# Kernel tuning notes

Hardware: AMD Instinct MI355X
Metric: run time of the kernel (lower is better)

The kernel has to match this reference:

```python
import jax, jax.numpy as jnp
import numpy as np

EMBED, HEAD, CTX = 1024, 64, 2048

def setup_inputs() -> dict:
    key = jax.random.key(0)
    k1, k2, k3, k4 = jax.random.split(key, 4)
    x = jax.random.normal(k1, (16, 2048, EMBED), dtype=jnp.float32)
    s = EMBED ** -0.5  # torch Linear default init scale-ish
    Wq = jax.random.normal(k2, (EMBED, HEAD), dtype=jnp.float32) * s
    Wk = jax.random.normal(k3, (EMBED, HEAD), dtype=jnp.float32) * s
    Wv = jax.random.normal(k4, (EMBED, HEAD), dtype=jnp.float32) * s
    return {"x": x, "Wq": Wq, "Wk": Wk, "Wv": Wv}

def reference(x, Wq, Wk, Wv):
    # x: [B, S, E] -> q,k,v: [B, S, H]
    q = jnp.einsum('bse,eh->bsh', x, Wq)
    k = jnp.einsum('bse,eh->bsh', x, Wk)
    v = jnp.einsum('bse,eh->bsh', x, Wv)
    scale = k.shape[-1] ** -0.5
    scores = jnp.einsum('bqh,bkh->bqk', q, k) * scale  # [B, S, S]
    S = x.shape[1]
    causal = jnp.tril(jnp.ones((S, S), dtype=bool))
    scores = jnp.where(causal, scores, -jnp.inf)
    attn = jax.nn.softmax(scores, axis=-1)
    return jnp.einsum('bqk,bkh->bqh', attn, v)  # [B, S, H]
```

## Files before the change

### kernel.cpp

```cpp
#include <hip/hip_runtime.h>
#include <math.h>

#define BATCH 16
#define SEQ   2048
#define EMB   1024
#define HD    64
#define NROWS (BATCH*SEQ)

typedef __attribute__((ext_vector_type(8))) short short8;
typedef __attribute__((ext_vector_type(4))) float f32x4;

#define SWZ(byte, row)   ((byte) ^ (((row) & 7) << 4))
#define SWZ16(byte, row) ((byte) ^ (((row) & 15) << 4))

__device__ __forceinline__ ushort f2bf(float f) {
    union { float f; unsigned u; } c; c.f = f;
    return (ushort)((c.u + 0x7FFF + ((c.u >> 16) & 1)) >> 16);
}

__device__ __forceinline__ void gload_lds16(const void* g, void* l) {
    __builtin_amdgcn_global_load_lds(
        (const __attribute__((address_space(1))) void*)g,
        (__attribute__((address_space(3))) void*)l, 16, 0, 0);
}

__global__ void k_transpose_w(const float* __restrict__ Wq,
                              const float* __restrict__ Wk,
                              const float* __restrict__ Wv,
                              ushort* __restrict__ wt) {
    int idx  = blockIdx.x * 256 + threadIdx.x;
    int c192 = idx >> 10;
    int e    = idx & 1023;
    const float* W = (c192 < 64) ? Wq : (c192 < 128 ? Wk : Wv);
    wt[idx] = f2bf(W[e * HD + (c192 & 63)]);
}

__global__ __launch_bounds__(256)
void k_qkv_proj(const float* __restrict__ x, const ushort* __restrict__ wt,
                ushort* __restrict__ qkv, ushort* __restrict__ vt) {
    __shared__ short8 smem[49152 / 16];
    char* base = (char*)smem;
    const int t = threadIdx.x, lane = t & 63, w = t >> 6;
    const int l15 = lane & 15, lg = lane >> 4;
    const int row0 = blockIdx.x * 64;
    const float* xrowp = x + (size_t)(row0 + w * 16 + l15) * EMB;

    f32x4 acc[12];
    #pragma unroll
    for (int mi = 0; mi < 12; ++mi) acc[mi] = (f32x4){0.f, 0.f, 0.f, 0.f};

    float4 xc[4], xn[4];

    auto stage_w = [&](int ch, int buf) {
        char* wb = base + buf * 24576;
        #pragma unroll
        for (int i = 0; i < 6; ++i) {
            int r = (w * 6 + i) * 8 + (lane >> 3);
            int j = (lane & 7) ^ (r & 7);
            gload_lds16(&wt[(size_t)r * EMB + ch * 64 + j * 8],
                        wb + (w * 6 + i) * 1024);
        }
    };
    auto load_x = [&](int ch, float4* xr) {
        #pragma unroll
        for (int s = 0; s < 2; ++s) {
            const float* p = xrowp + ch * 64 + s * 32 + lg * 8;
            xr[s * 2 + 0] = *(const float4*)(p);
            xr[s * 2 + 1] = *(const float4*)(p + 4);
        }
    };

    stage_w(0, 0); load_x(0, xc);
    #pragma unroll 2
    for (int ch = 0; ch < 16; ++ch) {
        int cur = ch & 1;
        if (ch < 15) {
            stage_w(ch + 1, cur ^ 1); load_x(ch + 1, xn);
            asm volatile("s_waitcnt vmcnt(10)" ::: "memory");
        } else {
            asm volatile("s_waitcnt vmcnt(0)" ::: "memory");
        }
        __builtin_amdgcn_sched_barrier(0);
        __builtin_amdgcn_s_barrier();
        char* wb = base + cur * 24576;
        #pragma unroll
        for (int s = 0; s < 2; ++s) {
            const float* xp = (const float*)&xc[s * 2];
            short8 xf;
            #pragma unroll
            for (int e = 0; e < 8; ++e) xf[e] = (short)f2bf(xp[e]);
            __builtin_amdgcn_s_setprio(1);
            #pragma unroll
            for (int mi = 0; mi < 12; ++mi) {
                int cr = mi * 16 + l15;
                short8 wf = *(short8*)(wb + SWZ(cr * 128 + s * 64 + lg * 16, cr));
                acc[mi] = (mi < 8)
                    ? __builtin_amdgcn_mfma_f32_16x16x32_bf16(wf, xf, acc[mi], 0, 0, 0)
                    : __builtin_amdgcn_mfma_f32_16x16x32_bf16(xf, wf, acc[mi], 0, 0, 0);
            }
            __builtin_amdgcn_s_setprio(0);
        }
        if (ch < 15) {
            #pragma unroll
            for (int i = 0; i < 4; ++i) xc[i] = xn[i];
        }
        __builtin_amdgcn_sched_barrier(0);
        __builtin_amdgcn_s_barrier();
    }

    char* qkb = base;
    char* vtb = base + 16384;
    const float qscale = 0.125f * 1.44269504f;
    #pragma unroll
    for (int mi = 0; mi < 12; ++mi) {
        ushort4 o;
        if (mi < 8) {
            float sc = (mi < 4) ? qscale : 1.0f;
            o.x = f2bf(acc[mi][0] * sc); o.y = f2bf(acc[mi][1] * sc);
            o.z = f2bf(acc[mi][2] * sc); o.w = f2bf(acc[mi][3] * sc);
            int xrow = w * 16 + l15, c = mi * 16 + lg * 4;
            *(ushort4*)(qkb + SWZ16(xrow * 256 + c * 2, xrow)) = o;
        } else {
            o.x = f2bf(acc[mi][0]); o.y = f2bf(acc[mi][1]);
            o.z = f2bf(acc[mi][2]); o.w = f2bf(acc[mi][3]);
            int hd = (mi - 8) * 16 + l15, key = w * 16 + lg * 4;
            *(ushort4*)(vtb + SWZ(hd * 128 + key * 2, hd)) = o;
        }
    }
    __syncthreads();
    const int b = row0 >> 11, r0b = row0 & 2047;
    #pragma unroll
    for (int i = 0; i < 4; ++i) {
        int idx = t + i * 256;
        int r = idx >> 4, g = idx & 15;
        short8 v = *(short8*)(qkb + SWZ16(r * 256 + g * 16, r));
        int c0 = g * 8, m = c0 >> 6, c = c0 & 63;
        *(short8*)&qkv[((size_t)m * NROWS + row0 + r) * HD + c] = v;
    }
    #pragma unroll
    for (int i = 0; i < 2; ++i) {
        int idx = t + i * 256;
        int hd = idx >> 3, g = idx & 7;
        short8 v = *(short8*)(vtb + SWZ(hd * 128 + g * 16, hd));
        *(short8*)&vt[((size_t)b * HD + hd) * SEQ + r0b + g * 8] = v;
    }
}

__global__ __launch_bounds__(256)
void k_attn(const ushort* __restrict__ q, const ushort* __restrict__ k,
            const ushort* __restrict__ vt, float* __restrict__ out) {
    __shared__ short8 smem[81920 / 16];
    char* base = (char*)smem;
    char* pls  = base + 65536;
    const int t = threadIdx.x, lane = t & 63, w = t >> 6;
    const int l15 = lane & 15, lg = lane >> 4;
    const int b = blockIdx.x & 15, qt = 31 - (blockIdx.x >> 4);
    const int row0 = qt * 64, r0w = row0 + w * 16;
    const ushort* qb = q  + (size_t)b * SEQ * HD;
    const ushort* kb = k  + (size_t)b * SEQ * HD;
    const ushort* vb = vt + (size_t)b * HD * SEQ;
    char* pw = pls + w * 4096;

    short8 qf[2];
    #pragma unroll
    for (int s = 0; s < 2; ++s)
        qf[s] = *(const short8*)&qb[(size_t)(r0w + l15) * HD + s * 32 + lg * 8];

    f32x4 oacc[4];
    #pragma unroll
    for (int h = 0; h < 4; ++h) oacc[h] = (f32x4){0.f, 0.f, 0.f, 0.f};
    float m_ = -INFINITY, l_ = 0.f;

    auto stage = [&](int kt, int buf) {
        char* kbuf = base + buf * 32768;
        char* vbuf = kbuf + 16384;
        int k0 = kt * 128;
        #pragma unroll
        for (int g = 0; g < 4; ++g) {
            int rk = w * 32 + g * 8 + (lane >> 3);
            int jk = (lane & 7) ^ (rk & 7);
            gload_lds16(&kb[(size_t)(k0 + rk) * HD + jk * 8],
                        kbuf + (w * 4 + g) * 1024);
            int rv = w * 16 + g * 4 + (lane >> 4);
            int jv = (lane & 15) ^ (rv & 15);
            gload_lds16(&vb[(size_t)rv * SEQ + k0 + jv * 8],
                        vbuf + (w * 4 + g) * 1024);
        }
    };

    const int npair = (qt + 2) >> 1;
    stage(0, 0);
    for (int kt = 0; kt < npair; ++kt) {
        int cur = kt & 1;
        if (kt + 1 < npair) {
            stage(kt + 1, cur ^ 1);
            asm volatile("s_waitcnt vmcnt(8)" ::: "memory");
        } else {
            asm volatile("s_waitcnt vmcnt(0)" ::: "memory");
        }
        __builtin_amdgcn_sched_barrier(0);
        __builtin_amdgcn_s_barrier();
        char* kls = base + cur * 32768;
        char* vls = kls + 16384;
        int k0 = kt * 128;

        f32x4 sa[8];
        #pragma unroll
        for (int a = 0; a < 8; ++a) sa[a] = (f32x4){0.f, 0.f, 0.f, 0.f};
        __builtin_amdgcn_s_setprio(1);
        #pragma unroll
        for (int s = 0; s < 2; ++s)
            #pragma unroll
            for (int a = 0; a < 8; ++a) {
                int r = a * 16 + l15;
                short8 kf = *(short8*)(kls + SWZ(r * 128 + s * 64 + lg * 16, r));
                sa[a] = __builtin_amdgcn_mfma_f32_16x16x32_bf16(kf, qf[s], sa[a], 0, 0, 0);
            }
        __builtin_amdgcn_s_setprio(0);

        if (kt == npair - 1) {
            int qrow = r0w + l15;
            #pragma unroll
            for (int a = 0; a < 8; ++a)
                #pragma unroll
                for (int r = 0; r < 4; ++r)
                    if (k0 + a * 16 + lg * 4 + r > qrow) sa[a][r] = -INFINITY;
        }

        float smax = -INFINITY;
        #pragma unroll
        for (int a = 0; a < 8; ++a)
            #pragma unroll
            for (int r = 0; r < 4; ++r) smax = fmaxf(smax, sa[a][r]);
        smax = fmaxf(smax, __shfl_xor(smax, 16));
        smax = fmaxf(smax, __shfl_xor(smax, 32));
        if (!__all(smax - m_ <= 8.0f)) {
            float mn   = fmaxf(m_, smax);
            float corr = __builtin_amdgcn_exp2f(m_ - mn);
            l_ *= corr;
            #pragma unroll
            for (int h = 0; h < 4; ++h) oacc[h] *= corr;
            m_ = mn;
        }
        float p[32], ps = 0.f;
        #pragma unroll
        for (int a = 0; a < 8; ++a)
            #pragma unroll
            for (int r = 0; r < 4; ++r) {
                float pv = __builtin_amdgcn_exp2f(sa[a][r] - m_);
                p[a * 4 + r] = pv; ps += pv;
            }
        ps += __shfl_xor(ps, 16);
        ps += __shfl_xor(ps, 32);
        l_ += ps;

        #pragma unroll
        for (int a = 0; a < 8; ++a) {
            ushort4 pb;
            pb.x = f2bf(p[a * 4 + 0]); pb.y = f2bf(p[a * 4 + 1]);
            pb.z = f2bf(p[a * 4 + 2]); pb.w = f2bf(p[a * 4 + 3]);
            *(ushort4*)(pw + SWZ16(l15 * 256 + a * 32 + lg * 8, l15)) = pb;
        }

        __builtin_amdgcn_s_setprio(1);
        #pragma unroll
        for (int ki = 0; ki < 4; ++ki) {
            short8 pf = *(short8*)(pw + SWZ16(l15 * 256 + ki * 64 + lg * 16, l15));
            #pragma unroll
            for (int h = 0; h < 4; ++h) {
                int rr = h * 16 + l15;
                short8 vf = *(short8*)(vls + SWZ16(rr * 256 + ki * 64 + lg * 16, rr));
                oacc[h] = __builtin_amdgcn_mfma_f32_16x16x32_bf16(vf, pf, oacc[h], 0, 0, 0);
            }
        }
        __builtin_amdgcn_s_setprio(0);
        __builtin_amdgcn_sched_barrier(0);
        __builtin_amdgcn_s_barrier();
    }

    float inv = 1.0f / l_;
    #pragma unroll
    for (int h = 0; h < 4; ++h) {
        f32x4 v = oacc[h] * inv;
        int qr = w * 16 + l15;
        *(f32x4*)(base + SWZ16(qr * 256 + h * 64 + lg * 16, qr)) = v;
    }
    __syncthreads();
    #pragma unroll
    for (int i = 0; i < 4; ++i) {
        int idx = t + i * 256;
        int r = idx >> 4, g = idx & 15;
        f32x4 v = *(f32x4*)(base + SWZ16(r * 256 + g * 16, r));
        *(f32x4*)&out[((size_t)b * SEQ + row0 + r) * HD + g * 4] = v;
    }
}

extern "C" void kernel_launch(void* const* d_in, const int* in_sizes, int n_in,
                              void* d_out, int out_size, void* d_ws, size_t ws_size,
                              hipStream_t stream) {
    const float* x  = (const float*)d_in[0];
    const float* Wq = (const float*)d_in[1];
    const float* Wk = (const float*)d_in[2];
    const float* Wv = (const float*)d_in[3];
    float* out = (float*)d_out;
    ushort* ws = (ushort*)d_ws;
    ushort* wt16 = ws;
    ushort* qk16 = ws + 192 * 1024;
    ushort* vt16 = qk16 + (size_t)2 * NROWS * HD;

    k_transpose_w<<<768, 256, 0, stream>>>(Wq, Wk, Wv, wt16);
    k_qkv_proj  <<<NROWS / 64, 256, 0, stream>>>(x, wt16, qk16, vt16);
    k_attn      <<<BATCH * (SEQ / 64), 256, 0, stream>>>(
                    qk16, qk16 + (size_t)NROWS * HD, vt16, out);
}
```

Baseline: 69.94 us.

## Split KV tile across wave pairs with 32-row query fragments and merge partial softmax

Each wave now owns 32 query rows and half of each 128-key tile, instead of 16 rows and the full tile. Every K fragment read from LDS therefore feeds two MFMAs, which halves K LDS reads per MFMA and roughly halves the P write and read traffic per wave. The two key-half partial results (running max, sum and output accumulator) are merged at the end through LDS. This adds a final merge step and doubles the accumulator register state per wave, which may hurt occupancy. The causal mask now uses a -1e30 running-max init, so a fully masked half-tile stays numerically safe.

Result: slower. 71.44 us (+2.1%).

```diff
diff --git a/kernel.cpp b/kernel.cpp
--- a/kernel.cpp
+++ b/kernel.cpp
@@ -146,6 +146,7 @@
     }
 }
 
+#define MINF (-1e30f)
 __global__ __launch_bounds__(256)
 void k_attn(const ushort* __restrict__ q, const ushort* __restrict__ k,
             const ushort* __restrict__ vt, float* __restrict__ out) {
@@ -154,22 +155,28 @@
     char* pls  = base + 65536;
     const int t = threadIdx.x, lane = t & 63, w = t >> 6;
     const int l15 = lane & 15, lg = lane >> 4;
+    const int rw = w & 1, kh = w >> 1;
     const int b = blockIdx.x & 15, qt = 31 - (blockIdx.x >> 4);
-    const int row0 = qt * 64, r0w = row0 + w * 16;
+    const int row0 = qt * 64;
     const ushort* qb = q  + (size_t)b * SEQ * HD;
     const ushort* kb = k  + (size_t)b * SEQ * HD;
     const ushort* vb = vt + (size_t)b * HD * SEQ;
     char* pw = pls + w * 4096;
 
-    short8 qf[2];
-    #pragma unroll
-    for (int s = 0; s < 2; ++s)
-        qf[s] = *(const short8*)&qb[(size_t)(r0w + l15) * HD + s * 32 + lg * 8];
-
-    f32x4 oacc[4];
-    #pragma unroll
-    for (int h = 0; h < 4; ++h) oacc[h] = (f32x4){0.f, 0.f, 0.f, 0.f};
-    float m_ = -INFINITY, l_ = 0.f;
+    short8 qf[2][2];
+    #pragma unroll
+    for (int f = 0; f < 2; ++f)
+        #pragma unroll
+        for (int s = 0; s < 2; ++s)
+            qf[f][s] = *(const short8*)&qb[(size_t)(row0 + rw * 32 + f * 16 + l15) * HD
+                                           + s * 32 + lg * 8];
+
+    f32x4 oacc[2][4];
+    #pragma unroll
+    for (int f = 0; f < 2; ++f)
+        #pragma unroll
+        for (int h = 0; h < 4; ++h) oacc[f][h] = (f32x4){0.f, 0.f, 0.f, 0.f};
+    float m_[2] = {MINF, MINF}, l_[2] = {0.f, 0.f};
 
     auto stage = [&](int kt, int buf) {
         char* kbuf = base + buf * 32768;
@@ -204,73 +211,89 @@
         char* vls = kls + 16384;
         int k0 = kt * 128;
 
-        f32x4 sa[8];
-        #pragma unroll
-        for (int a = 0; a < 8; ++a) sa[a] = (f32x4){0.f, 0.f, 0.f, 0.f};
+        f32x4 sa[2][4];
+        #pragma unroll
+        for (int f = 0; f < 2; ++f)
+            #pragma unroll
+            for (int a = 0; a < 4; ++a) sa[f][a] = (f32x4){0.f, 0.f, 0.f, 0.f};
         __builtin_amdgcn_s_setprio(1);
         #pragma unroll
         for (int s = 0; s < 2; ++s)
             #pragma unroll
-            for (int a = 0; a < 8; ++a) {
-                int r = a * 16 + l15;
+            for (int a = 0; a < 4; ++a) {
+                int r = kh * 64 + a * 16 + l15;
                 short8 kf = *(short8*)(kls + SWZ(r * 128 + s * 64 + lg * 16, r));
-                sa[a] = __builtin_amdgcn_mfma_f32_16x16x32_bf16(kf, qf[s], sa[a], 0, 0, 0);
+                sa[0][a] = __builtin_amdgcn_mfma_f32_16x16x32_bf16(kf, qf[0][s], sa[0][a], 0, 0, 0);
+                sa[1][a] = __builtin_amdgcn_mfma_f32_16x16x32_bf16(kf, qf[1][s], sa[1][a], 0, 0, 0);
             }
         __builtin_amdgcn_s_setprio(0);
 
         if (kt == npair - 1) {
-            int qrow = r0w + l15;
-            #pragma unroll
-            for (int a = 0; a < 8; ++a)
+            #pragma unroll
+            for (int f = 0; f < 2; ++f) {
+                int qrow = row0 + rw * 32 + f * 16 + l15;
+                #pragma unroll
+                for (int a = 0; a < 4; ++a)
+                    #pragma unroll
+                    for (int r = 0; r < 4; ++r)
+                        if (k0 + kh * 64 + a * 16 + lg * 4 + r > qrow)
+                            sa[f][a][r] = -INFINITY;
+            }
+        }
+
+        #pragma unroll
+        for (int f = 0; f < 2; ++f) {
+            float ma[4];
+            #pragma unroll
+            for (int a = 0; a < 4; ++a)
+                ma[a] = fmaxf(fmaxf(sa[f][a][0], sa[f][a][1]),
+                              fmaxf(sa[f][a][2], sa[f][a][3]));
+            float mx = fmaxf(fmaxf(ma[0], ma[1]), fmaxf(ma[2], ma[3]));
+            mx = fmaxf(mx, __shfl_xor(mx, 16));
+            mx = fmaxf(mx, __shfl_xor(mx, 32));
+            if (!__all(mx - m_[f] <= 8.0f)) {
+                float mn   = fmaxf(m_[f], mx);
+                float corr = __builtin_amdgcn_exp2f(m_[f] - mn);
+                l_[f] *= corr;
+                #pragma unroll
+                for (int h = 0; h < 4; ++h) oacc[f][h] *= corr;
+                m_[f] = mn;
+            }
+            float p[16];
+            #pragma unroll
+            for (int a = 0; a < 4; ++a)
                 #pragma unroll
                 for (int r = 0; r < 4; ++r)
-                    if (k0 + a * 16 + lg * 4 + r > qrow) sa[a][r] = -INFINITY;
-        }
-
-        float smax = -INFINITY;
-        #pragma unroll
-        for (int a = 0; a < 8; ++a)
-            #pragma unroll
-            for (int r = 0; r < 4; ++r) smax = fmaxf(smax, sa[a][r]);
-        smax = fmaxf(smax, __shfl_xor(smax, 16));
-        smax = fmaxf(smax, __shfl_xor(smax, 32));
-        if (!__all(smax - m_ <= 8.0f)) {
-            float mn   = fmaxf(m_, smax);
-            float corr = __builtin_amdgcn_exp2f(m_ - mn);
-            l_ *= corr;
-            #pragma unroll
-            for (int h = 0; h < 4; ++h) oacc[h] *= corr;
-            m_ = mn;
-        }
-        float p[32], ps = 0.f;
-        #pragma unroll
-        for (int a = 0; a < 8; ++a)
-            #pragma unroll
-            for (int r = 0; r < 4; ++r) {
-                float pv = __builtin_amdgcn_exp2f(sa[a][r] - m_);
-                p[a * 4 + r] = pv; ps += pv;
-            }
-        ps += __shfl_xor(ps, 16);
-        ps += __shfl_xor(ps, 32);
-        l_ += ps;
-
-        #pragma unroll
-        for (int a = 0; a < 8; ++a) {
-            ushort4 pb;
-            pb.x = f2bf(p[a * 4 + 0]); pb.y = f2bf(p[a * 4 + 1]);
-            pb.z = f2bf(p[a * 4 + 2]); pb.w = f2bf(p[a * 4 + 3]);
-            *(ushort4*)(pw + SWZ16(l15 * 256 + a * 32 + lg * 8, l15)) = pb;
+                    p[a * 4 + r] = __builtin_amdgcn_exp2f(sa[f][a][r] - m_[f]);
+            float s01 = (p[0] + p[1]) + (p[2] + p[3]);
+            float s23 = (p[4] + p[5]) + (p[6] + p[7]);
+            float s45 = (p[8] + p[9]) + (p[10] + p[11]);
+            float s67 = (p[12] + p[13]) + (p[14] + p[15]);
+            float ps = (s01 + s23) + (s45 + s67);
+            ps += __shfl_xor(ps, 16);
+            ps += __shfl_xor(ps, 32);
+            l_[f] += ps;
+            #pragma unroll
+            for (int a = 0; a < 4; ++a) {
+                ushort4 pb;
+                pb.x = f2bf(p[a * 4 + 0]); pb.y = f2bf(p[a * 4 + 1]);
+                pb.z = f2bf(p[a * 4 + 2]); pb.w = f2bf(p[a * 4 + 3]);
+                int prow = f * 16 + l15;
+                *(ushort4*)(pw + SWZ(prow * 128 + a * 32 + lg * 8, prow)) = pb;
+            }
         }
 
         __builtin_amdgcn_s_setprio(1);
         #pragma unroll
-        for (int ki = 0; ki < 4; ++ki) {
-            short8 pf = *(short8*)(pw + SWZ16(l15 * 256 + ki * 64 + lg * 16, l15));
+        for (int ki = 0; ki < 2; ++ki) {
+            short8 pf0 = *(short8*)(pw + SWZ((0 * 16 + l15) * 128 + ki * 64 + lg * 16, 0 * 16 + l15));
+            short8 pf1 = *(short8*)(pw + SWZ((1 * 16 + l15) * 128 + ki * 64 + lg * 16, 1 * 16 + l15));
             #pragma unroll
             for (int h = 0; h < 4; ++h) {
                 int rr = h * 16 + l15;
-                short8 vf = *(short8*)(vls + SWZ16(rr * 256 + ki * 64 + lg * 16, rr));
-                oacc[h] = __builtin_amdgcn_mfma_f32_16x16x32_bf16(vf, pf, oacc[h], 0, 0, 0);
+                short8 vf = *(short8*)(vls + SWZ16(rr * 256 + kh * 128 + ki * 64 + lg * 16, rr));
+                oacc[0][h] = __builtin_amdgcn_mfma_f32_16x16x32_bf16(vf, pf0, oacc[0][h], 0, 0, 0);
+                oacc[1][h] = __builtin_amdgcn_mfma_f32_16x16x32_bf16(vf, pf1, oacc[1][h], 0, 0, 0);
             }
         }
         __builtin_amdgcn_s_setprio(0);
@@ -278,20 +301,36 @@
         __builtin_amdgcn_s_barrier();
     }
 
-    float inv = 1.0f / l_;
-    #pragma unroll
-    for (int h = 0; h < 4; ++h) {
-        f32x4 v = oacc[h] * inv;
-        int qr = w * 16 + l15;
-        *(f32x4*)(base + SWZ16(qr * 256 + h * 64 + lg * 16, qr)) = v;
+    char* obuf = base + rw * 8192;
+    float* ml  = (float*)(base + 16384 + rw * 256);
+    if (kh == 1) {
+        #pragma unroll
+        for (int f = 0; f < 2; ++f) {
+            int prow = f * 16 + l15;
+            #pragma unroll
+            for (int h = 0; h < 4; ++h)
+                *(f32x4*)(obuf + SWZ16(prow * 256 + (h * 16 + lg * 4) * 4, prow)) = oacc[f][h];
+            if (lg == 0) { ml[prow] = m_[f]; ml[32 + prow] = l_[f]; }
+        }
     }
     __syncthreads();
-    #pragma unroll
-    for (int i = 0; i < 4; ++i) {
-        int idx = t + i * 256;
-        int r = idx >> 4, g = idx & 15;
-        f32x4 v = *(f32x4*)(base + SWZ16(r * 256 + g * 16, r));
-        *(f32x4*)&out[((size_t)b * SEQ + row0 + r) * HD + g * 4] = v;
+    if (kh == 0) {
+        #pragma unroll
+        for (int f = 0; f < 2; ++f) {
+            int prow = f * 16 + l15;
+            float m2 = ml[prow], l2 = ml[32 + prow];
+            float M  = fmaxf(m_[f], m2);
+            float s1 = __builtin_amdgcn_exp2f(m_[f] - M);
+            float s2 = __builtin_amdgcn_exp2f(m2 - M);
+            float inv = 1.0f / (l_[f] * s1 + l2 * s2);
+            int qrow = row0 + rw * 32 + prow;
+            #pragma unroll
+            for (int h = 0; h < 4; ++h) {
+                f32x4 o2 = *(f32x4*)(obuf + SWZ16(prow * 256 + (h * 16 + lg * 4) * 4, prow));
+                f32x4 o  = (oacc[f][h] * s1 + o2 * s2) * inv;
+                *(f32x4*)&out[((size_t)b * SEQ + qrow) * HD + h * 16 + lg * 4] = o;
+            }
+        }
     }
 }
 
```
